# Kernel tuning notes

Measured on AMD Instinct MI355X. Metric: run time of the kernel, lower is better.

Reference implementation:

```python
import jax, jax.numpy as jnp
import numpy as np

B, S, R, H = 32, 512, 196, 1024


def setup_inputs() -> dict:
    key = jax.random.key(0)
    ks = jax.random.split(key, 12)
    sc = 1.0 / np.sqrt(H)
    return {
        "dns_feature": jax.random.normal(ks[0], (B, S, H), jnp.float32),
        "img_features": jax.random.normal(ks[1], (B, R, H), jnp.float32),
        # attention 1 params (dns_linear_1 has bias, img_linear_1 does not)
        "W_d1": jax.random.normal(ks[2], (H, H), jnp.float32) * sc,
        "b_d1": jax.random.normal(ks[3], (H,), jnp.float32) * sc,
        "W_i1": jax.random.normal(ks[4], (H, H), jnp.float32) * sc,
        "w_att1": jax.random.normal(ks[5], (2 * H,), jnp.float32) * sc,
        "b_att1": jax.random.normal(ks[6], (), jnp.float32) * sc,
        # attention 2 params (img_linear_2 has bias, dns_linear_2 does not)
        "W_d2": jax.random.normal(ks[7], (H, H), jnp.float32) * sc,
        "W_i2": jax.random.normal(ks[8], (H, H), jnp.float32) * sc,
        "b_i2": jax.random.normal(ks[9], (H,), jnp.float32) * sc,
        "w_att2": jax.random.normal(ks[10], (2 * H,), jnp.float32) * sc,
        "b_att2": jax.random.normal(ks[11], (), jnp.float32) * sc,
    }


def reference(dns_feature, img_features, W_d1, b_d1, W_i1, w_att1, b_att1,
              W_d2, W_i2, b_i2, w_att2, b_att2):
    h = dns_feature.shape[-1]
    # --- attention 1: dns attends over image regions ---
    # original: tanh(concat(Lin(dns_rep), Lin(img_rep))) -> att_linear_1.
    # tanh is elementwise and the concat linear is separable, so
    # score[b,s,r] = wA . tanh(W_d1 dns[b,s] + b_d1) + wB . tanh(W_i1 img[b,r]) + b_att1
    dns_p = jnp.tanh(jnp.einsum('bsh,oh->bso', dns_feature, W_d1) + b_d1)   # (B,S,H)
    img_p = jnp.tanh(jnp.einsum('brh,oh->bro', img_features, W_i1))          # (B,R,H)
    wA, wB = w_att1[:h], w_att1[h:]
    scores1 = (jnp.einsum('bsh,h->bs', dns_p, wA)[:, :, None]
               + jnp.einsum('brh,h->br', img_p, wB)[:, None, :] + b_att1)    # (B,S,R)
    visual_att = jax.nn.softmax(scores1, axis=-1)
    att_img_features = jnp.einsum('bsr,brh->bsh', visual_att, img_features)  # (B,S,H)
    # --- attention 2: attended image (per token i) attends over dns tokens j ---
    # concat order is [img_proj, dns_proj] here.
    img_p2 = jnp.tanh(jnp.einsum('bih,oh->bio', att_img_features, W_i2) + b_i2)  # (B,S,H)
    dns_p2 = jnp.tanh(jnp.einsum('bjh,oh->bjo', dns_feature, W_d2))              # (B,S,H)
    wI, wD = w_att2[:h], w_att2[h:]
    scores2 = (jnp.einsum('bih,h->bi', img_p2, wI)[:, :, None]
               + jnp.einsum('bjh,h->bj', dns_p2, wD)[:, None, :] + b_att2)       # (B,S,S)
    textual_att = jax.nn.softmax(scores2, axis=-1)
    att_dns_features = jnp.einsum('bij,bjh->bih', textual_att, dns_feature)      # (B,S,H)
    return att_dns_features, att_img_features
```

## Files before the change

kernel.cpp:

```cpp
#include <hip/hip_runtime.h>
#include <hip/hip_bf16.h>
#include <stdint.h>

typedef __bf16 bh;
typedef __bf16 bf16x8 __attribute__((ext_vector_type(8)));
typedef float f32x4 __attribute__((ext_vector_type(4)));
typedef unsigned int u32;

#define B_  32
#define S_  512
#define R_  196
#define H_  1024
#define BH  (B_ * H_)


__device__ __forceinline__ float fast_tanh(float x) {
  x = fminf(10.f, fmaxf(-10.f, x));
  float e = __expf(2.f * x);
  return (e - 1.f) / (e + 1.f);
}

__device__ __forceinline__ bf16x8 cvt8(const float4 a, const float4 b) {
  bf16x8 r;
  r[0] = (bh)a.x; r[1] = (bh)a.y; r[2] = (bh)a.z; r[3] = (bh)a.w;
  r[4] = (bh)b.x; r[5] = (bh)b.y; r[6] = (bh)b.z; r[7] = (bh)b.w;
  return r;
}


__global__ __launch_bounds__(256, 2)
void score_gemm_kernel(const float* __restrict__ dns, const float* __restrict__ img,
                       const float* __restrict__ Wd2, const float* __restrict__ Wi1,
                       const float* __restrict__ watt1, const float* __restrict__ watt2,
                       float* __restrict__ sPartD, float* __restrict__ sPartB) {
  __shared__ __align__(16) bh As[128 * 32];
  __shared__ __align__(16) bh Bs[128 * 32];
  __shared__ float sred[128];

  const int tid = threadIdx.x;
  const int wave = tid >> 6, lane = tid & 63;
  const int bx = blockIdx.x, ny = blockIdx.y;

  const float* X; const float* W; const float* w; float* sp; int m0;
  if (bx < 128) { X = dns; W = Wd2; w = watt2 + H_; sp = sPartD; m0 = bx * 128; }
  else          { X = img; W = Wi1; w = watt1 + H_; sp = sPartB; m0 = (bx - 128) * 128; }
  const int n0 = ny * 128;

  const int r0  = tid >> 2;
  const int r1  = r0 + 64;
  const int seg = (tid & 3) * 8;

  const float* Ag0 = X + ((size_t)(m0 + r0) * H_ + seg);
  const float* Ag1 = X + ((size_t)(m0 + r1) * H_ + seg);
  const float* Bg0 = W + ((size_t)(n0 + r0) * H_ + seg);
  const float* Bg1 = W + ((size_t)(n0 + r1) * H_ + seg);

  bh* Al0 = As + r0 * 32 + seg;
  bh* Al1 = As + r1 * 32 + seg;
  bh* Bl0 = Bs + r0 * 32 + seg;
  bh* Bl1 = Bs + r1 * 32 + seg;

  const int wm = wave >> 1, wn = wave & 1;
  const int col = lane & 15, quad = lane >> 4;

  f32x4 acc[4][4] = {};

  float4 qa00 = *(const float4*)(Ag0),     qa01 = *(const float4*)(Ag0 + 4);
  float4 qa10 = *(const float4*)(Ag1),     qa11 = *(const float4*)(Ag1 + 4);
  float4 qb00 = *(const float4*)(Bg0),     qb01 = *(const float4*)(Bg0 + 4);
  float4 qb10 = *(const float4*)(Bg1),     qb11 = *(const float4*)(Bg1 + 4);

  for (int kt = 0; kt < 32; ++kt) {
    if (kt) __syncthreads();
    *(bf16x8*)Al0 = cvt8(qa00, qa01);
    *(bf16x8*)Al1 = cvt8(qa10, qa11);
    *(bf16x8*)Bl0 = cvt8(qb00, qb01);
    *(bf16x8*)Bl1 = cvt8(qb10, qb11);
    if (kt + 1 < 32) {
      const int ko = (kt + 1) * 32;
      qa00 = *(const float4*)(Ag0 + ko); qa01 = *(const float4*)(Ag0 + ko + 4);
      qa10 = *(const float4*)(Ag1 + ko); qa11 = *(const float4*)(Ag1 + ko + 4);
      qb00 = *(const float4*)(Bg0 + ko); qb01 = *(const float4*)(Bg0 + ko + 4);
      qb10 = *(const float4*)(Bg1 + ko); qb11 = *(const float4*)(Bg1 + ko + 4);
    }
    __syncthreads();

    bf16x8 af[4], bfr[4];
#pragma unroll
    for (int mi = 0; mi < 4; ++mi)
      af[mi] = *(const bf16x8*)(As + (wm * 64 + mi * 16 + col) * 32 + quad * 8);
#pragma unroll
    for (int ni = 0; ni < 4; ++ni)
      bfr[ni] = *(const bf16x8*)(Bs + (wn * 64 + ni * 16 + col) * 32 + quad * 8);

#pragma unroll
    for (int mi = 0; mi < 4; ++mi)
#pragma unroll
      for (int ni = 0; ni < 4; ++ni)
        acc[mi][ni] = __builtin_amdgcn_mfma_f32_16x16x32_bf16(af[mi], bfr[ni], acc[mi][ni], 0, 0, 0);
  }

  float wv[4];
#pragma unroll
  for (int ni = 0; ni < 4; ++ni) wv[ni] = w[n0 + wn * 64 + ni * 16 + col];

  float ppv[4][4];
#pragma unroll
  for (int mi = 0; mi < 4; ++mi) {
#pragma unroll
    for (int reg = 0; reg < 4; ++reg) {
      float pp = 0.f;
#pragma unroll
      for (int ni = 0; ni < 4; ++ni) pp += fast_tanh(acc[mi][ni][reg]) * wv[ni];
      pp += __shfl_xor(pp, 1);
      pp += __shfl_xor(pp, 2);
      pp += __shfl_xor(pp, 4);
      pp += __shfl_xor(pp, 8);
      ppv[mi][reg] = pp;
    }
  }

  if (wn == 0 && col == 0) {
#pragma unroll
    for (int mi = 0; mi < 4; ++mi)
#pragma unroll
      for (int reg = 0; reg < 4; ++reg)
        sred[wm * 64 + mi * 16 + quad * 4 + reg] = ppv[mi][reg];
  }
  __syncthreads();
  if (wn == 1 && col == 0) {
#pragma unroll
    for (int mi = 0; mi < 4; ++mi)
#pragma unroll
      for (int reg = 0; reg < 4; ++reg) {
        int ml = wm * 64 + mi * 16 + quad * 4 + reg;
        sp[(size_t)(m0 + ml) * 8 + ny] = sred[ml] + ppv[mi][reg];
      }
  }
}

__global__ __launch_bounds__(512)
void softmax_kernel(const float* __restrict__ sPartD, const float* __restrict__ sPartB,
                    float* __restrict__ q, float* __restrict__ p) {
  __shared__ float red[8];
  const int b = blockIdx.x, tid = threadIdx.x;
  const int wave = tid >> 6, lane = tid & 63;

  {
    const float4* p4 = (const float4*)(sPartD + (size_t)(b * S_ + tid) * 8);
    float4 x0 = p4[0], x1 = p4[1];
    float x = x0.x + x0.y + x0.z + x0.w + x1.x + x1.y + x1.z + x1.w;
    float wm = x;
#pragma unroll
    for (int msk = 32; msk; msk >>= 1) wm = fmaxf(wm, __shfl_xor(wm, msk));
    if (!lane) red[wave] = wm;
    __syncthreads();
    float bm = red[0];
#pragma unroll
    for (int i = 1; i < 8; ++i) bm = fmaxf(bm, red[i]);
    __syncthreads();
    float e = __expf(x - bm);
    float ws = e;
#pragma unroll
    for (int msk = 32; msk; msk >>= 1) ws += __shfl_xor(ws, msk);
    if (!lane) red[wave] = ws;
    __syncthreads();
    float bs = 0.f;
#pragma unroll
    for (int i = 0; i < 8; ++i) bs += red[i];
    q[b * S_ + tid] = e / bs;
    __syncthreads();
  }
  {
    float x = -3.0e38f;
    if (tid < R_) {
      const float4* p4 = (const float4*)(sPartB + (size_t)(b * R_ + tid) * 8);
      float4 x0 = p4[0], x1 = p4[1];
      x = x0.x + x0.y + x0.z + x0.w + x1.x + x1.y + x1.z + x1.w;
    }
    float wm = x;
#pragma unroll
    for (int msk = 32; msk; msk >>= 1) wm = fmaxf(wm, __shfl_xor(wm, msk));
    if (!lane) red[wave] = wm;
    __syncthreads();
    float bm = red[0];
#pragma unroll
    for (int i = 1; i < 8; ++i) bm = fmaxf(bm, red[i]);
    __syncthreads();
    float e = (tid < R_) ? __expf(x - bm) : 0.f;
    float ws = e;
#pragma unroll
    for (int msk = 32; msk; msk >>= 1) ws += __shfl_xor(ws, msk);
    if (!lane) red[wave] = ws;
    __syncthreads();
    float bs = 0.f;
#pragma unroll
    for (int i = 0; i < 8; ++i) bs += red[i];
    if (tid < R_) p[b * R_ + tid] = e / bs;
  }
}

__global__ __launch_bounds__(256)
void wsum_kernel(const float* __restrict__ dns, const float* __restrict__ img,
                 const float* __restrict__ q, const float* __restrict__ p,
                 float* __restrict__ uPart, float* __restrict__ vPart) {
  __shared__ float qs[64];
  const int b = blockIdx.x, tid = threadIdx.x;
  const int zc = blockIdx.y;
  const float* X; const float* wq; float* outp; int J, j0, jn;
  if (zc < 8) { X = dns; wq = q; outp = uPart + zc * BH;       J = S_; j0 = zc * 64;       jn = 64; }
  else        { X = img; wq = p; outp = vPart + (zc - 8) * BH; J = R_; j0 = (zc - 8) * 49; jn = 49; }
  if (tid < jn) qs[tid] = wq[b * J + j0 + tid];
  __syncthreads();
  const int h = tid * 4;
  float4 a = {0.f, 0.f, 0.f, 0.f};
  for (int jj = 0; jj < jn; ++jj) {
    float4 xv = *(const float4*)(X + ((size_t)(b * J + j0 + jj) * H_ + h));
    float qv = qs[jj];
    a.x += qv * xv.x; a.y += qv * xv.y; a.z += qv * xv.z; a.w += qv * xv.w;
  }
  *(float4*)(outp + (size_t)b * H_ + h) = a;
}

__global__ __launch_bounds__(256)
void combine_kernel(const float* __restrict__ uPart, const float* __restrict__ vPart,
                    float* __restrict__ u, float* __restrict__ v) {
  const int b = blockIdx.x, tid = threadIdx.x;
  const int i = b * 256 + tid;
  float4 a = {0.f, 0.f, 0.f, 0.f};
#pragma unroll
  for (int c = 0; c < 8; ++c) {
    float4 s = ((const float4*)(uPart + (size_t)c * BH))[i];
    a.x += s.x; a.y += s.y; a.z += s.z; a.w += s.w;
  }
  ((float4*)u)[i] = a;
  float4 cacc = {0.f, 0.f, 0.f, 0.f};
#pragma unroll
  for (int c = 0; c < 4; ++c) {
    float4 s = ((const float4*)(vPart + (size_t)c * BH))[i];
    cacc.x += s.x; cacc.y += s.y; cacc.z += s.z; cacc.w += s.w;
  }
  ((float4*)v)[i] = cacc;
}

__global__ __launch_bounds__(256)
void bcast_kernel(const float* __restrict__ u, const float* __restrict__ v,
                  float* __restrict__ out) {
  const int PER4 = B_ * S_ * H_ / 4;
  const int t = blockIdx.x * 256 + threadIdx.x;
  const int which = (t >= PER4);
  const int r = t - which * PER4;
  const int b = r >> 17;
  const int h4 = r & 255;
  const float4 val = ((const float4*)((which ? v : u) + (size_t)b * H_))[h4];
  ((float4*)out)[t] = val;
}


extern "C" void kernel_launch(void* const* d_in, const int* in_sizes, int n_in,
                              void* d_out, int out_size, void* d_ws, size_t ws_size,
                              hipStream_t stream) {
  const float* dns   = (const float*)d_in[0];
  const float* img   = (const float*)d_in[1];
  const float* Wi1   = (const float*)d_in[4];
  const float* watt1 = (const float*)d_in[5];
  const float* Wd2   = (const float*)d_in[7];
  const float* watt2 = (const float*)d_in[10];
  float* out = (float*)d_out;

  float* ws = (float*)d_ws;
  float* sPartD = ws;
  float* sPartB = ws + 131072;
  float* q      = ws + 181248;
  float* p      = ws + 197632;
  float* uPart  = ws + 203904;
  float* vPart  = ws + 466048;
  float* u      = ws + 597120;
  float* v      = ws + 629888;

  score_gemm_kernel<<<dim3(128 + 49, 8), 256, 0, stream>>>(
      dns, img, Wd2, Wi1, watt1, watt2, sPartD, sPartB);
  softmax_kernel<<<B_, 512, 0, stream>>>(sPartD, sPartB, q, p);
  wsum_kernel<<<dim3(B_, 12), 256, 0, stream>>>(dns, img, q, p, uPart, vPart);
  combine_kernel<<<B_, 256, 0, stream>>>(uPart, vPart, u, v);
  bcast_kernel<<<32768, 256, 0, stream>>>(u, v, out);
}
```

Before: 341.1 us.

## Pre-convert GEMM operands to bf16 and stream via direct global-to-LDS loads

Adds a separate conversion pass that writes dns, img and both weight matrices as bf16. The score GEMM then loads tiles with global_load_lds straight into shared memory, which removes per-iteration register staging and fp32-to-bf16 conversion, and its grid order is swapped so the weight tiles for one row block run together. The wsum kernel is split into more chunks for more parallelism, and combine now sums 16 partials. The cost is an extra full read and write pass over the inputs, and the GEMM loses its register prefetch overlap because loads are issued right before the barrier.

```diff
diff --git a/kernel.cpp b/kernel.cpp
--- a/kernel.cpp
+++ b/kernel.cpp
@@ -27,10 +27,39 @@
   return r;
 }
 
-
-__global__ __launch_bounds__(256, 2)
-void score_gemm_kernel(const float* __restrict__ dns, const float* __restrict__ img,
-                       const float* __restrict__ Wd2, const float* __restrict__ Wi1,
+__device__ __forceinline__ void gload_lds16(const bh* g, bh* l) {
+  __builtin_amdgcn_global_load_lds(
+      (__attribute__((address_space(1))) void*)g,
+      (__attribute__((address_space(3))) void*)l,
+      16, 0, 0);
+}
+
+#define G_DNS 2097152
+#define G_IMG 802816
+#define G_W   131072
+#define G_TOT (G_DNS + G_IMG + 2 * G_W)
+
+__global__ __launch_bounds__(256)
+void convert_kernel(const float* __restrict__ dns, const float* __restrict__ img,
+                    const float* __restrict__ Wd2, const float* __restrict__ Wi1,
+                    bh* __restrict__ dnsB, bh* __restrict__ imgB,
+                    bh* __restrict__ wd2B, bh* __restrict__ wi1B) {
+  for (int g = blockIdx.x * 256 + threadIdx.x; g < G_TOT; g += gridDim.x * 256) {
+    const float* src; bh* dst; int off;
+    if (g < G_DNS)                  { src = dns; dst = dnsB; off = g; }
+    else if (g < G_DNS + G_IMG)     { src = img; dst = imgB; off = g - G_DNS; }
+    else if (g < G_DNS + G_IMG + G_W) { src = Wd2; dst = wd2B; off = g - G_DNS - G_IMG; }
+    else                            { src = Wi1; dst = wi1B; off = g - G_DNS - G_IMG - G_W; }
+    float4 a = ((const float4*)src)[(size_t)off * 2];
+    float4 b = ((const float4*)src)[(size_t)off * 2 + 1];
+    ((bf16x8*)dst)[off] = cvt8(a, b);
+  }
+}
+
+
+__global__ __launch_bounds__(256, 3)
+void score_gemm_kernel(const bh* __restrict__ dnsB, const bh* __restrict__ imgB,
+                       const bh* __restrict__ Wd2B, const bh* __restrict__ Wi1B,
                        const float* __restrict__ watt1, const float* __restrict__ watt2,
                        float* __restrict__ sPartD, float* __restrict__ sPartB) {
   __shared__ __align__(16) bh As[128 * 32];
@@ -39,50 +68,32 @@
 
   const int tid = threadIdx.x;
   const int wave = tid >> 6, lane = tid & 63;
-  const int bx = blockIdx.x, ny = blockIdx.y;
-
-  const float* X; const float* W; const float* w; float* sp; int m0;
-  if (bx < 128) { X = dns; W = Wd2; w = watt2 + H_; sp = sPartD; m0 = bx * 128; }
-  else          { X = img; W = Wi1; w = watt1 + H_; sp = sPartB; m0 = (bx - 128) * 128; }
+  const int ny = blockIdx.x, my = blockIdx.y;
+
+  const bh* X; const bh* W; const float* w; float* sp; int m0;
+  if (my < 128) { X = dnsB; W = Wd2B; w = watt2 + H_; sp = sPartD; m0 = my * 128; }
+  else          { X = imgB; W = Wi1B; w = watt1 + H_; sp = sPartB; m0 = (my - 128) * 128; }
   const int n0 = ny * 128;
 
-  const int r0  = tid >> 2;
-  const int r1  = r0 + 64;
-  const int seg = (tid & 3) * 8;
-
-  const float* Ag0 = X + ((size_t)(m0 + r0) * H_ + seg);
-  const float* Ag1 = X + ((size_t)(m0 + r1) * H_ + seg);
-  const float* Bg0 = W + ((size_t)(n0 + r0) * H_ + seg);
-  const float* Bg1 = W + ((size_t)(n0 + r1) * H_ + seg);
-
-  bh* Al0 = As + r0 * 32 + seg;
-  bh* Al1 = As + r1 * 32 + seg;
-  bh* Bl0 = Bs + r0 * 32 + seg;
-  bh* Bl1 = Bs + r1 * 32 + seg;
+  const int srow = wave * 32 + (lane >> 2);
+  const int sseg = (lane & 3) * 8;
+  const bh* Ag = X + ((size_t)(m0 + srow) * H_ + sseg);
+  const bh* Bg = W + ((size_t)(n0 + srow) * H_ + sseg);
+  bh* Al = As + (wave * 32) * 32;
+  bh* Bl = Bs + (wave * 32) * 32;
 
   const int wm = wave >> 1, wn = wave & 1;
   const int col = lane & 15, quad = lane >> 4;
 
   f32x4 acc[4][4] = {};
 
-  float4 qa00 = *(const float4*)(Ag0),     qa01 = *(const float4*)(Ag0 + 4);
-  float4 qa10 = *(const float4*)(Ag1),     qa11 = *(const float4*)(Ag1 + 4);
-  float4 qb00 = *(const float4*)(Bg0),     qb01 = *(const float4*)(Bg0 + 4);
-  float4 qb10 = *(const float4*)(Bg1),     qb11 = *(const float4*)(Bg1 + 4);
-
   for (int kt = 0; kt < 32; ++kt) {
     if (kt) __syncthreads();
-    *(bf16x8*)Al0 = cvt8(qa00, qa01);
-    *(bf16x8*)Al1 = cvt8(qa10, qa11);
-    *(bf16x8*)Bl0 = cvt8(qb00, qb01);
-    *(bf16x8*)Bl1 = cvt8(qb10, qb11);
-    if (kt + 1 < 32) {
-      const int ko = (kt + 1) * 32;
-      qa00 = *(const float4*)(Ag0 + ko); qa01 = *(const float4*)(Ag0 + ko + 4);
-      qa10 = *(const float4*)(Ag1 + ko); qa11 = *(const float4*)(Ag1 + ko + 4);
-      qb00 = *(const float4*)(Bg0 + ko); qb01 = *(const float4*)(Bg0 + ko + 4);
-      qb10 = *(const float4*)(Bg1 + ko); qb11 = *(const float4*)(Bg1 + ko + 4);
-    }
+    const int ko = kt * 32;
+    gload_lds16(Ag + ko,              Al);
+    gload_lds16(Ag + ko + 16 * H_,    Al + 16 * 32);
+    gload_lds16(Bg + ko,              Bl);
+    gload_lds16(Bg + ko + 16 * H_,    Bl + 16 * 32);
     __syncthreads();
 
     bf16x8 af[4], bfr[4];
@@ -205,21 +216,34 @@
                  const float* __restrict__ q, const float* __restrict__ p,
                  float* __restrict__ uPart, float* __restrict__ vPart) {
   __shared__ float qs[64];
-  const int b = blockIdx.x, tid = threadIdx.x;
-  const int zc = blockIdx.y;
-  const float* X; const float* wq; float* outp; int J, j0, jn;
-  if (zc < 8) { X = dns; wq = q; outp = uPart + zc * BH;       J = S_; j0 = zc * 64;       jn = 64; }
-  else        { X = img; wq = p; outp = vPart + (zc - 8) * BH; J = R_; j0 = (zc - 8) * 49; jn = 49; }
-  if (tid < jn) qs[tid] = wq[b * J + j0 + tid];
-  __syncthreads();
+  const int b = blockIdx.x, tid = threadIdx.x, zc = blockIdx.y;
   const int h = tid * 4;
   float4 a = {0.f, 0.f, 0.f, 0.f};
-  for (int jj = 0; jj < jn; ++jj) {
-    float4 xv = *(const float4*)(X + ((size_t)(b * J + j0 + jj) * H_ + h));
-    float qv = qs[jj];
-    a.x += qv * xv.x; a.y += qv * xv.y; a.z += qv * xv.z; a.w += qv * xv.w;
-  }
-  *(float4*)(outp + (size_t)b * H_ + h) = a;
+  if (zc < 16) {
+    const int j0 = zc * 32;
+    if (tid < 32) qs[tid] = q[b * S_ + j0 + tid];
+    __syncthreads();
+    const float* Xb = dns + ((size_t)(b * S_ + j0) * H_ + h);
+#pragma unroll
+    for (int jj = 0; jj < 32; ++jj) {
+      float4 xv = *(const float4*)(Xb + (size_t)jj * H_);
+      float qv = qs[jj];
+      a.x += qv * xv.x; a.y += qv * xv.y; a.z += qv * xv.z; a.w += qv * xv.w;
+    }
+    *(float4*)(uPart + (size_t)zc * BH + (size_t)b * H_ + h) = a;
+  } else {
+    const int j0 = (zc - 16) * 49;
+    if (tid < 49) qs[tid] = p[b * R_ + j0 + tid];
+    __syncthreads();
+    const float* Xb = img + ((size_t)(b * R_ + j0) * H_ + h);
+#pragma unroll
+    for (int jj = 0; jj < 49; ++jj) {
+      float4 xv = *(const float4*)(Xb + (size_t)jj * H_);
+      float qv = qs[jj];
+      a.x += qv * xv.x; a.y += qv * xv.y; a.z += qv * xv.z; a.w += qv * xv.w;
+    }
+    *(float4*)(vPart + (size_t)(zc - 16) * BH + (size_t)b * H_ + h) = a;
+  }
 }
 
 __global__ __launch_bounds__(256)
@@ -229,7 +253,7 @@
   const int i = b * 256 + tid;
   float4 a = {0.f, 0.f, 0.f, 0.f};
 #pragma unroll
-  for (int c = 0; c < 8; ++c) {
+  for (int c = 0; c < 16; ++c) {
     float4 s = ((const float4*)(uPart + (size_t)c * BH))[i];
     a.x += s.x; a.y += s.y; a.z += s.z; a.w += s.w;
   }
@@ -274,14 +298,19 @@
   float* q      = ws + 181248;
   float* p      = ws + 197632;
   float* uPart  = ws + 203904;
-  float* vPart  = ws + 466048;
-  float* u      = ws + 597120;
-  float* v      = ws + 629888;
-
-  score_gemm_kernel<<<dim3(128 + 49, 8), 256, 0, stream>>>(
-      dns, img, Wd2, Wi1, watt1, watt2, sPartD, sPartB);
+  float* vPart  = ws + 728192;
+  float* u      = ws + 859264;
+  float* v      = ws + 892032;
+  bh* dnsB = (bh*)(ws + 924800);
+  bh* imgB = (bh*)(ws + 9313408);
+  bh* wd2B = (bh*)(ws + 12524672);
+  bh* wi1B = (bh*)(ws + 13048960);
+
+  convert_kernel<<<2048, 256, 0, stream>>>(dns, img, Wd2, Wi1, dnsB, imgB, wd2B, wi1B);
+  score_gemm_kernel<<<dim3(8, 128 + 49), 256, 0, stream>>>(
+      dnsB, imgB, wd2B, wi1B, watt1, watt2, sPartD, sPartB);
   softmax_kernel<<<B_, 512, 0, stream>>>(sPartD, sPartB, q, p);
-  wsum_kernel<<<dim3(B_, 12), 256, 0, stream>>>(dns, img, q, p, uPart, vPart);
+  wsum_kernel<<<dim3(B_, 20), 256, 0, stream>>>(dns, img, q, p, uPart, vPart);
   combine_kernel<<<B_, 256, 0, stream>>>(uPart, vPart, u, v);
   bcast_kernel<<<32768, 256, 0, stream>>>(u, v, out);
 }
```

Result: faster. 330.9 us (-3.0%).
